# Performance work log

Measured on AMD Instinct MI355X. Metric: run time of the kernel, lower is better.

## Reference

```python
import jax, jax.numpy as jnp
import numpy as np
import math

B, L, H, N, OUT, NPRED, NCTRL = 16, 4096, 512, 64, 256, 128, 64


def setup_inputs() -> dict:
    key = jax.random.key(0)
    ks = jax.random.split(key, 12)
    Nh = N // 2
    inp = jax.random.normal(ks[0], (B, L, H), dtype=jnp.float32)
    spec = jax.random.normal(ks[1], (B, L, NCTRL), dtype=jnp.float32)
    # S4DKernel params
    C = jax.random.normal(ks[2], (H, Nh, 2), dtype=jnp.float32)  # view_as_real of cfloat C
    log_dt = (jax.random.uniform(ks[3], (H,), dtype=jnp.float32)
              * (math.log(0.1) - math.log(0.001)) + math.log(0.001))
    log_A_real = jnp.log(0.5 * jnp.ones((H, Nh), dtype=jnp.float32))
    A_imag = math.pi * jnp.broadcast_to(jnp.arange(Nh, dtype=jnp.float32), (H, Nh))
    D = jax.random.normal(ks[4], (H,), dtype=jnp.float32)
    # output_linear: Conv1d(H, 2H, 1) then GLU(dim=-2)
    conv_w = jax.random.normal(ks[5], (2 * H, H), dtype=jnp.float32) / np.sqrt(H)
    conv_b = jax.random.normal(ks[6], (2 * H,), dtype=jnp.float32) * 0.01
    # output: Linear(in_len, out_len) applied on length axis
    out_w = jax.random.normal(ks[7], (OUT, L), dtype=jnp.float32) / np.sqrt(L)
    out_b = jax.random.normal(ks[8], (OUT,), dtype=jnp.float32) * 0.01
    return {"inp": inp, "spec": spec, "C": C, "log_dt": log_dt,
            "log_A_real": log_A_real, "A_imag": A_imag, "D": D,
            "conv_w": conv_w, "conv_b": conv_b, "out_w": out_w, "out_b": out_b}


def s4d_kernel(C, log_dt, log_A_real, A_imag, L):
    # Materialize SSM convolution kernel K: (H, L)
    dt = jnp.exp(log_dt)                                  # (H,)
    Cc = C[..., 0] + 1j * C[..., 1]                       # (H, N/2) complex
    A = -jnp.exp(log_A_real) + 1j * A_imag                # (H, N/2)
    dtA = A * dt[:, None]                                 # (H, N/2)
    # Vandermonde: exp(dtA * l) for l in [0, L)
    V = jnp.exp(dtA[:, :, None] * jnp.arange(L, dtype=jnp.float32))  # (H, N/2, L)
    Cc = Cc * (jnp.exp(dtA) - 1.0) / A                    # (H, N/2)
    K = 2.0 * jnp.einsum('hn,hnl->hl', Cc, V).real        # (H, L)
    return K


def reference(inp, spec, C, log_dt, log_A_real, A_imag, D, conv_w, conv_b, out_w, out_b):
    x = jnp.swapaxes(inp, -1, -2)                         # (B, H, L)
    Lx = x.shape[-1]
    k = s4d_kernel(C, log_dt, log_A_real, A_imag, Lx)     # (H, L)
    # FFT long convolution (linear conv via zero-padding to 2L)
    k_f = jnp.fft.rfft(k, n=2 * Lx)                       # (H, L+1)
    x_f = jnp.fft.rfft(x, n=2 * Lx)                       # (B, H, L+1)
    y = jnp.fft.irfft(x_f * k_f, n=2 * Lx)[..., :Lx]      # (B, H, L)
    y = y + x * D[:, None]                                # skip connection
    y = jax.nn.gelu(y, approximate=False)                 # torch nn.GELU default (erf)
    # Conv1d(k=1) + GLU over channel dim
    z = jnp.einsum('oh,bhl->bol', conv_w, y) + conv_b[:, None]  # (B, 2H, L)
    a, b = z[:, :H, :], z[:, H:, :]
    y = a * jax.nn.sigmoid(b)                             # (B, H, L)
    # Linear over length axis: L -> OUT
    y = jnp.einsum('bhl,ol->bho', y, out_w) + out_b       # (B, H, OUT)
    y = jnp.swapaxes(y, -1, -2)                           # (B, OUT, H)
    return y[:, :OUT, -NPRED:]
```

## Files before the change

kernel.cpp:

```cpp
#include <hip/hip_runtime.h>
#include <hip/hip_bf16.h>
#include <math.h>

#define B_     16
#define L_     4096
#define H_     512
#define NH     32
#define OUT_   256
#define NPRED_ 128
#define CCH    8
#define LCH    512

typedef __attribute__((ext_vector_type(8))) short bf16x8;
typedef __attribute__((ext_vector_type(4))) float f32x4;
typedef __attribute__((ext_vector_type(2))) float f32x2;

__global__ void prep_kernel(const float* __restrict__ conv_w, const float* __restrict__ conv_b,
                            const float* __restrict__ out_w,
                            __hip_bfloat16* __restrict__ Wsel, float* __restrict__ bselp,
                            __hip_bfloat16* __restrict__ outw)
{
    int idx = blockIdx.x * blockDim.x + threadIdx.x;
    if (idx < 256 * 512) {
        int r = idx >> 9, hcol = idx & 511;
        int src = (r < 128) ? (384 + r) : (768 + r);
        Wsel[idx] = __float2bfloat16(conv_w[src * H_ + hcol]);
    } else if (idx < 256 * 512 + 256 * 4096) {
        int i2 = idx - 256 * 512;
        outw[i2] = __float2bfloat16(out_w[i2]);
    } else if (idx < 256 * 512 + 256 * 4096 + 256) {
        int r = idx - 256 * 512 - 256 * 4096;
        int src = (r < 128) ? (384 + r) : (768 + r);
        bselp[r] = conv_b[src];
    }
}

__global__ __launch_bounds__(256)
void scan_pass1(const float* __restrict__ inp, const float* __restrict__ log_dt,
                const float* __restrict__ log_A_real, const float* __restrict__ A_imag,
                float2* __restrict__ M)
{
    const int b = blockIdx.x, hg = blockIdx.y, cq = blockIdx.z;
    const int tid = threadIdx.x;
    const int wv = tid >> 6, lane = tid & 63;
    const int c = cq * 4 + wv;
    const int hl = lane & 15, nb = (lane >> 4) * 8;
    const int h = hg * 16 + hl;

    f32x2 WR[4], WI[4], WIN[4], SR[4], SI[4];
    const float dt = expf(log_dt[h]);
#pragma unroll
    for (int g = 0; g < 4; ++g) {
#pragma unroll
        for (int e = 0; e < 2; ++e) {
            const int n = nb + g * 2 + e;
            const float Ar = -expf(log_A_real[h * NH + n]);
            const float Ai = A_imag[h * NH + n];
            const float er = expf(Ar * dt);
            WR[g][e] = er * cosf(Ai * dt);
            WI[g][e] = er * sinf(Ai * dt);
            WIN[g][e] = -WI[g][e];
        }
        SR[g] = (f32x2){0.f, 0.f};
        SI[g] = (f32x2){0.f, 0.f};
    }

    const float* xp = inp + ((size_t)b * L_ + (size_t)c * LCH) * H_ + h;
    float xq0 = xp[0 * (size_t)H_];
    float xq1 = xp[1 * (size_t)H_];
    float xq2 = xp[2 * (size_t)H_];
    float xq3 = xp[3 * (size_t)H_];

#define P1_STEP(XV)                                                            \
    {                                                                          \
        const f32x2 X = (f32x2){(XV), (XV)};                                   \
        _Pragma("unroll")                                                      \
        for (int g = 0; g < 4; ++g) {                                          \
            f32x2 t   = __builtin_elementwise_fma(WIN[g], SI[g], X);           \
            f32x2 nSR = __builtin_elementwise_fma(WR[g], SR[g], t);            \
            f32x2 u   = WI[g] * SR[g];                                         \
            f32x2 nSI = __builtin_elementwise_fma(WR[g], SI[g], u);            \
            SR[g] = nSR; SI[g] = nSI;                                          \
        }                                                                      \
    }

#pragma unroll 4
    for (int l = 0; l < LCH - 4; ++l) {
        const float xf = xp[(size_t)(l + 4) * H_];
        P1_STEP(xq0);
        xq0 = xq1; xq1 = xq2; xq2 = xq3; xq3 = xf;
    }
#pragma unroll
    for (int l = LCH - 4; l < LCH; ++l) {
        P1_STEP(xq0);
        xq0 = xq1; xq1 = xq2; xq2 = xq3;
    }
#undef P1_STEP

    float2* Mp = M + (((size_t)b * CCH + c) * H_ + h) * NH + nb;
#pragma unroll
    for (int g = 0; g < 4; ++g) {
        float4 v; v.x = SR[g][0]; v.y = SI[g][0]; v.z = SR[g][1]; v.w = SI[g][1];
        *(float4*)&Mp[g * 2] = v;
    }
}

__global__ __launch_bounds__(256)
void scan_pass2(const float* __restrict__ log_dt, const float* __restrict__ log_A_real,
                const float* __restrict__ A_imag, float2* __restrict__ M)
{
    const int idx = blockIdx.x * 256 + threadIdx.x;
    const int n = idx & 31, h = (idx >> 5) & 511, b = idx >> 14;
    const float dt = expf(log_dt[h]);
    const float Ar = -expf(log_A_real[h * NH + n]);
    const float Ai = A_imag[h * NH + n];
    const float er = expf(Ar * dt);
    float wr = er * cosf(Ai * dt), wi = er * sinf(Ai * dt);
#pragma unroll
    for (int s = 0; s < 9; ++s) {
        float nr = wr * wr - wi * wi;
        float ni = 2.0f * wr * wi;
        wr = nr; wi = ni;
    }
    float sre = 0.f, sim = 0.f;
#pragma unroll
    for (int c = 0; c < CCH; ++c) {
        const size_t mi_ = (((size_t)b * CCH + c) * H_ + h) * NH + n;
        float2 m = M[mi_];
        M[mi_] = make_float2(sre, sim);
        float nr = fmaf(wr, sre, fmaf(-wi, sim, m.x));
        float ni = fmaf(wr, sim, fmaf(wi, sre, m.y));
        sre = nr; sim = ni;
    }
}

__global__ __launch_bounds__(256)
void scan_pass3(const float* __restrict__ inp, const float* __restrict__ C,
                const float* __restrict__ log_dt, const float* __restrict__ log_A_real,
                const float* __restrict__ A_imag, const float* __restrict__ Dv,
                const float2* __restrict__ Sin, __hip_bfloat16* __restrict__ gT)
{
    const int b = blockIdx.x, hg = blockIdx.y, cq = blockIdx.z;
    const int tid = threadIdx.x;
    const int wv = tid >> 6, lane = tid & 63;
    const int c = cq * 4 + wv;
    const int hl = lane & 15, nb = (lane >> 4) * 8;
    const int h = hg * 16 + hl;

    f32x2 WR[4], WI[4], WIN[4], CR[4], CNI[4], SR[4], SI[4];
    const float dt = expf(log_dt[h]);
    const float2* Sp = Sin + (((size_t)b * CCH + c) * H_ + h) * NH + nb;
#pragma unroll
    for (int g = 0; g < 4; ++g) {
#pragma unroll
        for (int e = 0; e < 2; ++e) {
            const int n = nb + g * 2 + e;
            const float Ar = -expf(log_A_real[h * NH + n]);
            const float Ai = A_imag[h * NH + n];
            const float er = expf(Ar * dt);
            const float wrr = er * cosf(Ai * dt);
            const float wii = er * sinf(Ai * dt);
            const float m2 = Ar * Ar + Ai * Ai;
            const float nr = wrr - 1.0f, nim = wii;
            const float qr = (nr * Ar + nim * Ai) / m2;
            const float qi = (nim * Ar - nr * Ai) / m2;
            const float Crv = C[(h * NH + n) * 2 + 0];
            const float Civ = C[(h * NH + n) * 2 + 1];
            WR[g][e] = wrr;  WI[g][e] = wii;  WIN[g][e] = -wii;
            CR[g][e]  =  2.0f * (Crv * qr - Civ * qi);
            CNI[g][e] = -2.0f * (Crv * qi + Civ * qr);
            float2 sv = Sp[g * 2 + e];
            SR[g][e] = sv.x; SI[g][e] = sv.y;
        }
    }
    const float Dh = Dv[h];

    const float* xp = inp + ((size_t)b * L_ + (size_t)c * LCH) * H_ + h;
    __hip_bfloat16* gp = gT + ((size_t)b * L_ + (size_t)c * LCH) * H_ + h;

    float xq0 = xp[0 * (size_t)H_];
    float xq1 = xp[1 * (size_t)H_];
    float xq2 = xp[2 * (size_t)H_];
    float xq3 = xp[3 * (size_t)H_];

#define P3_STEP(LV, XV)                                                        \
    {                                                                          \
        const f32x2 X = (f32x2){(XV), (XV)};                                   \
        f32x2 yp = (f32x2){0.f, 0.f};                                          \
        _Pragma("unroll")                                                      \
        for (int g = 0; g < 4; ++g) {                                          \
            f32x2 t   = __builtin_elementwise_fma(WIN[g], SI[g], X);           \
            f32x2 nSR = __builtin_elementwise_fma(WR[g], SR[g], t);            \
            f32x2 u   = WI[g] * SR[g];                                         \
            f32x2 nSI = __builtin_elementwise_fma(WR[g], SI[g], u);            \
            SR[g] = nSR; SI[g] = nSI;                                          \
            yp = __builtin_elementwise_fma(CR[g], nSR, yp);                    \
            yp = __builtin_elementwise_fma(CNI[g], nSI, yp);                   \
        }                                                                      \
        float y = yp[0] + yp[1];                                               \
        y += __shfl_xor(y, 16);                                                \
        y += __shfl_xor(y, 32);                                                \
        const float v = fmaf(Dh, (XV), y);                                     \
        float u2 = v * fmaf(0.0356774081f, v * v, 0.797884561f);               \
        u2 = fmaxf(u2, -15.0f);                                                \
        const float e2 = __expf(-2.0f * u2);                                   \
        const float th = 1.0f - 2.0f * e2 * __builtin_amdgcn_rcpf(1.0f + e2);  \
        const float ge = 0.5f * v * (1.0f + th);                               \
        if (lane < 16) gp[(size_t)(LV) * H_] = __float2bfloat16(ge);           \
    }

#pragma unroll 2
    for (int l = 0; l < LCH - 4; ++l) {
        const float xf = xp[(size_t)(l + 4) * H_];
        P3_STEP(l, xq0);
        xq0 = xq1; xq1 = xq2; xq2 = xq3; xq3 = xf;
    }
#pragma unroll
    for (int l = LCH - 4; l < LCH; ++l) {
        P3_STEP(l, xq0);
        xq0 = xq1; xq1 = xq2; xq2 = xq3;
    }
#undef P3_STEP
}

__device__ __forceinline__ unsigned short bf16bits(float f) {
    __hip_bfloat16 hv = __float2bfloat16(f);
    return *reinterpret_cast<unsigned short*>(&hv);
}

__global__ __launch_bounds__(512)
void gemm1_kernel(const __hip_bfloat16* __restrict__ gT, const __hip_bfloat16* __restrict__ Wsel,
                  const float* __restrict__ bsel, __hip_bfloat16* __restrict__ gated)
{
    const int b  = blockIdx.y;
    const int l0 = blockIdx.x * 128;
    const int tid = threadIdx.x;
    const int wid = tid >> 6, lane = tid & 63;
    const int wrr = wid >> 2;
    const int wcc = wid & 3;
    const int lr  = lane & 15;
    const int lk8 = (lane >> 4) * 8;

    __shared__ short As[128][40];
    __shared__ short Bs[256][40];

    f32x4 acc[4][4];
#pragma unroll
    for (int i = 0; i < 4; ++i)
#pragma unroll
        for (int j = 0; j < 4; ++j) acc[i][j] = (f32x4){0.f, 0.f, 0.f, 0.f};

    const short* gsrc = (const short*)gT + ((size_t)b * L_ + l0) * H_;
    const short* wsrc = (const short*)Wsel;
    const int arow = tid >> 2, aseg = tid & 3;

    for (int ks = 0; ks < 16; ++ks) {
        const int k0 = ks * 32;
        uint4 av  = *(const uint4*)(gsrc + (size_t)arow * H_ + k0 + aseg * 8);
        uint4 bv0 = *(const uint4*)(wsrc + (size_t)arow * 512 + k0 + aseg * 8);
        uint4 bv1 = *(const uint4*)(wsrc + (size_t)(arow + 128) * 512 + k0 + aseg * 8);
        *(uint4*)&As[arow][aseg * 8]       = av;
        *(uint4*)&Bs[arow][aseg * 8]       = bv0;
        *(uint4*)&Bs[arow + 128][aseg * 8] = bv1;
        __syncthreads();

        bf16x8 af[4], bfr[4];
#pragma unroll
        for (int mi = 0; mi < 4; ++mi)
            af[mi] = *(const bf16x8*)&As[wrr * 64 + mi * 16 + lr][lk8];
#pragma unroll
        for (int ni = 0; ni < 4; ++ni) {
            int col = (ni < 2) ? (wcc * 32 + ni * 16) : (128 + wcc * 32 + (ni - 2) * 16);
            bfr[ni] = *(const bf16x8*)&Bs[col + lr][lk8];
        }
#pragma unroll
        for (int mi = 0; mi < 4; ++mi)
#pragma unroll
            for (int ni = 0; ni < 4; ++ni)
                acc[mi][ni] = __builtin_amdgcn_mfma_f32_16x16x32_bf16(af[mi], bfr[ni], acc[mi][ni], 0, 0, 0);
        __syncthreads();
    }

    const int lj4 = (lane >> 4) * 4;
#pragma unroll
    for (int mi = 0; mi < 4; ++mi) {
#pragma unroll
        for (int ni = 0; ni < 2; ++ni) {
            const int oa = wcc * 32 + ni * 16 + lr;
            const float ba  = bsel[oa];
            const float bbv = bsel[oa + 128];
            ushort4 pack;
            unsigned short* pu = (unsigned short*)&pack;
#pragma unroll
            for (int j = 0; j < 4; ++j) {
                float za = acc[mi][ni][j] + ba;
                float zb = acc[mi][ni + 2][j] + bbv;
                float gv = za * (1.0f / (1.0f + expf(-zb)));
                pu[j] = bf16bits(gv);
            }
            const int lrow = l0 + wrr * 64 + mi * 16 + lj4;
            *(ushort4*)((unsigned short*)gated + ((size_t)b * NPRED_ + oa) * L_ + lrow) = pack;
        }
    }
}

__global__ __launch_bounds__(256)
void gemm2_kernel(const __hip_bfloat16* __restrict__ gated, const __hip_bfloat16* __restrict__ outw,
                  const float* __restrict__ outb, float* __restrict__ outp)
{
    const int b  = blockIdx.y;
    const int ot = blockIdx.x & 3, ht = blockIdx.x >> 2;
    const int o0 = ot * 64, hh0 = ht * 64;
    const int tid = threadIdx.x;
    const int wid = tid >> 6, lane = tid & 63;
    const int wrr = wid >> 1;
    const int wcc = wid & 1;
    const int lr  = lane & 15;
    const int lk8 = (lane >> 4) * 8;

    __shared__ short As[64][72];
    __shared__ short Bs[64][72];

    f32x4 acc[2][2];
#pragma unroll
    for (int i = 0; i < 2; ++i)
#pragma unroll
        for (int j = 0; j < 2; ++j) acc[i][j] = (f32x4){0.f, 0.f, 0.f, 0.f};

    const short* asrc = (const short*)gated + ((size_t)b * NPRED_ + hh0) * L_;
    const short* bsrc = (const short*)outw + (size_t)o0 * L_;
    const int row = tid >> 2, seg = tid & 3;

    for (int ks = 0; ks < 64; ++ks) {
        const int k0 = ks * 64;
        uint4 a0 = *(const uint4*)(asrc + (size_t)row * L_ + k0 + seg * 8);
        uint4 a1 = *(const uint4*)(asrc + (size_t)row * L_ + k0 + 32 + seg * 8);
        uint4 b0 = *(const uint4*)(bsrc + (size_t)row * L_ + k0 + seg * 8);
        uint4 b1 = *(const uint4*)(bsrc + (size_t)row * L_ + k0 + 32 + seg * 8);
        __syncthreads();
        *(uint4*)&As[row][seg * 8]      = a0;
        *(uint4*)&As[row][32 + seg * 8] = a1;
        *(uint4*)&Bs[row][seg * 8]      = b0;
        *(uint4*)&Bs[row][32 + seg * 8] = b1;
        __syncthreads();

#pragma unroll
        for (int kk = 0; kk < 2; ++kk) {
            bf16x8 af[2], bfv[2];
#pragma unroll
            for (int mi = 0; mi < 2; ++mi)
                af[mi] = *(const bf16x8*)&As[wrr * 32 + mi * 16 + lr][kk * 32 + lk8];
#pragma unroll
            for (int ni = 0; ni < 2; ++ni)
                bfv[ni] = *(const bf16x8*)&Bs[wcc * 32 + ni * 16 + lr][kk * 32 + lk8];
#pragma unroll
            for (int mi = 0; mi < 2; ++mi)
#pragma unroll
                for (int ni = 0; ni < 2; ++ni)
                    acc[mi][ni] = __builtin_amdgcn_mfma_f32_16x16x32_bf16(af[mi], bfv[ni], acc[mi][ni], 0, 0, 0);
        }
    }

    const int lj4 = (lane >> 4) * 4;
#pragma unroll
    for (int mi = 0; mi < 2; ++mi) {
#pragma unroll
        for (int ni = 0; ni < 2; ++ni) {
            const int og = o0 + wcc * 32 + ni * 16 + lr;
            const float bo = outb[og];
            float4 v;
            v.x = acc[mi][ni][0] + bo;
            v.y = acc[mi][ni][1] + bo;
            v.z = acc[mi][ni][2] + bo;
            v.w = acc[mi][ni][3] + bo;
            const int hh = hh0 + wrr * 32 + mi * 16 + lj4;
            *(float4*)(outp + ((size_t)b * OUT_ + og) * NPRED_ + hh) = v;
        }
    }
}

extern "C" void kernel_launch(void* const* d_in, const int* in_sizes, int n_in,
                              void* d_out, int out_size, void* d_ws, size_t ws_size,
                              hipStream_t stream)
{
    const float* inp        = (const float*)d_in[0];
    const float* C          = (const float*)d_in[2];
    const float* log_dt     = (const float*)d_in[3];
    const float* log_A_real = (const float*)d_in[4];
    const float* A_imag     = (const float*)d_in[5];
    const float* Dv         = (const float*)d_in[6];
    const float* conv_w     = (const float*)d_in[7];
    const float* conv_b     = (const float*)d_in[8];
    const float* out_w      = (const float*)d_in[9];
    const float* out_b      = (const float*)d_in[10];
    float* outp = (float*)d_out;

    const size_t off_Wsel  = 0;
    const size_t off_outw  = 262144;
    const size_t off_bsel  = 2359296;
    const size_t off_gT    = 2360320;
    const size_t off_gated = 69469184;
    const size_t off_M     = off_gated;
    const size_t need      = 86246400;
    if (ws_size < need) return;

    char* ws = (char*)d_ws;
    __hip_bfloat16* Wsel  = (__hip_bfloat16*)(ws + off_Wsel);
    __hip_bfloat16* outw  = (__hip_bfloat16*)(ws + off_outw);
    float*          bselp = (float*)(ws + off_bsel);
    __hip_bfloat16* gT    = (__hip_bfloat16*)(ws + off_gT);
    __hip_bfloat16* gated = (__hip_bfloat16*)(ws + off_gated);
    float2*         M     = (float2*)(ws + off_M);

    const int prep_total = 256 * 512 + 256 * 4096 + 256;
    prep_kernel<<<(prep_total + 255) / 256, 256, 0, stream>>>(conv_w, conv_b, out_w, Wsel, bselp, outw);
    scan_pass1<<<dim3(16, 32, 2), 256, 0, stream>>>(inp, log_dt, log_A_real, A_imag, M);
    scan_pass2<<<1024, 256, 0, stream>>>(log_dt, log_A_real, A_imag, M);
    scan_pass3<<<dim3(16, 32, 2), 256, 0, stream>>>(inp, C, log_dt, log_A_real, A_imag, Dv, M, gT);
    gemm1_kernel<<<dim3(32, 16), 512, 0, stream>>>(gT, Wsel, bselp, gated);
    gemm2_kernel<<<dim3(8, 16), 256, 0, stream>>>(gated, outw, out_b, outp);
}
```

Baseline: 580.3 us.

## Force packed FMA via inline asm and block scan steps with distributed GELU epilogue

Rewrites the inner recurrence of scan passes 1 and 3 to use inline-asm v_pk_fma_f32/v_pk_mul_f32 so the compiler cannot scalarize the packed complex updates. The input stream is now prefetched in blocks of 8 timesteps into registers instead of a 4-deep rolling queue. In pass 3, the cross-lane shuffle reductions are batched over 8 steps, and the GELU epilogue and stores are spread across all four 16-lane groups (each handling two timesteps) rather than only lane<16 doing the work. The cost is higher register pressure from the 16 buffered inputs and 8 partial sums, plus inline asm that hides instructions from the compiler's scheduler.

```diff
diff --git a/kernel.cpp b/kernel.cpp
--- a/kernel.cpp
+++ b/kernel.cpp
@@ -14,6 +14,10 @@
 typedef __attribute__((ext_vector_type(8))) short bf16x8;
 typedef __attribute__((ext_vector_type(4))) float f32x4;
 typedef __attribute__((ext_vector_type(2))) float f32x2;
+
+#define PKFMA(D, A, Bv, Cv) asm("v_pk_fma_f32 %0, %1, %2, %3" : "=v"(D) : "v"(A), "v"(Bv), "v"(Cv))
+#define PKFMA_ACC(D, A, Bv) asm("v_pk_fma_f32 %0, %1, %2, %0" : "+v"(D) : "v"(A), "v"(Bv))
+#define PKMUL(D, A, Bv)     asm("v_pk_mul_f32 %0, %1, %2" : "=v"(D) : "v"(A), "v"(Bv))
 
 __global__ void prep_kernel(const float* __restrict__ conv_w, const float* __restrict__ conv_b,
                             const float* __restrict__ out_w,
@@ -66,34 +70,34 @@
     }
 
     const float* xp = inp + ((size_t)b * L_ + (size_t)c * LCH) * H_ + h;
-    float xq0 = xp[0 * (size_t)H_];
-    float xq1 = xp[1 * (size_t)H_];
-    float xq2 = xp[2 * (size_t)H_];
-    float xq3 = xp[3 * (size_t)H_];
+
+    float xc[8], xn[8];
+#pragma unroll
+    for (int i = 0; i < 8; ++i) xc[i] = xp[(size_t)i * H_];
 
 #define P1_STEP(XV)                                                            \
     {                                                                          \
-        const f32x2 X = (f32x2){(XV), (XV)};                                   \
+        f32x2 X; X[0] = (XV); X[1] = (XV);                                     \
         _Pragma("unroll")                                                      \
         for (int g = 0; g < 4; ++g) {                                          \
-            f32x2 t   = __builtin_elementwise_fma(WIN[g], SI[g], X);           \
-            f32x2 nSR = __builtin_elementwise_fma(WR[g], SR[g], t);            \
-            f32x2 u   = WI[g] * SR[g];                                         \
-            f32x2 nSI = __builtin_elementwise_fma(WR[g], SI[g], u);            \
+            f32x2 t1, t2, nSR, nSI;                                            \
+            PKFMA(t1, WIN[g], SI[g], X);                                       \
+            PKFMA(nSR, WR[g], SR[g], t1);                                      \
+            PKMUL(t2, WI[g], SR[g]);                                           \
+            PKFMA(nSI, WR[g], SI[g], t2);                                      \
             SR[g] = nSR; SI[g] = nSI;                                          \
         }                                                                      \
     }
 
-#pragma unroll 4
-    for (int l = 0; l < LCH - 4; ++l) {
-        const float xf = xp[(size_t)(l + 4) * H_];
-        P1_STEP(xq0);
-        xq0 = xq1; xq1 = xq2; xq2 = xq3; xq3 = xf;
-    }
-#pragma unroll
-    for (int l = LCH - 4; l < LCH; ++l) {
-        P1_STEP(xq0);
-        xq0 = xq1; xq1 = xq2; xq2 = xq3;
+    for (int blk = 0; blk < 64; ++blk) {
+        if (blk < 63) {
+#pragma unroll
+            for (int i = 0; i < 8; ++i) xn[i] = xp[(size_t)(blk * 8 + 8 + i) * H_];
+        }
+#pragma unroll
+        for (int s = 0; s < 8; ++s) P1_STEP(xc[s]);
+#pragma unroll
+        for (int i = 0; i < 8; ++i) xc[i] = xn[i];
     }
 #undef P1_STEP
 
@@ -146,6 +150,9 @@
     const int c = cq * 4 + wv;
     const int hl = lane & 15, nb = (lane >> 4) * 8;
     const int h = hg * 16 + hl;
+    const bool pb0 = ((lane >> 4) & 1) != 0;
+    const bool pb1 = ((lane >> 4) & 2) != 0;
+    const int p = lane >> 4;
 
     f32x2 WR[4], WI[4], WIN[4], CR[4], CNI[4], SR[4], SI[4];
     const float dt = expf(log_dt[h]);
@@ -178,49 +185,60 @@
     const float* xp = inp + ((size_t)b * L_ + (size_t)c * LCH) * H_ + h;
     __hip_bfloat16* gp = gT + ((size_t)b * L_ + (size_t)c * LCH) * H_ + h;
 
-    float xq0 = xp[0 * (size_t)H_];
-    float xq1 = xp[1 * (size_t)H_];
-    float xq2 = xp[2 * (size_t)H_];
-    float xq3 = xp[3 * (size_t)H_];
-
-#define P3_STEP(LV, XV)                                                        \
-    {                                                                          \
-        const f32x2 X = (f32x2){(XV), (XV)};                                   \
-        f32x2 yp = (f32x2){0.f, 0.f};                                          \
-        _Pragma("unroll")                                                      \
-        for (int g = 0; g < 4; ++g) {                                          \
-            f32x2 t   = __builtin_elementwise_fma(WIN[g], SI[g], X);           \
-            f32x2 nSR = __builtin_elementwise_fma(WR[g], SR[g], t);            \
-            f32x2 u   = WI[g] * SR[g];                                         \
-            f32x2 nSI = __builtin_elementwise_fma(WR[g], SI[g], u);            \
-            SR[g] = nSR; SI[g] = nSI;                                          \
-            yp = __builtin_elementwise_fma(CR[g], nSR, yp);                    \
-            yp = __builtin_elementwise_fma(CNI[g], nSI, yp);                   \
-        }                                                                      \
-        float y = yp[0] + yp[1];                                               \
-        y += __shfl_xor(y, 16);                                                \
-        y += __shfl_xor(y, 32);                                                \
-        const float v = fmaf(Dh, (XV), y);                                     \
-        float u2 = v * fmaf(0.0356774081f, v * v, 0.797884561f);               \
-        u2 = fmaxf(u2, -15.0f);                                                \
-        const float e2 = __expf(-2.0f * u2);                                   \
-        const float th = 1.0f - 2.0f * e2 * __builtin_amdgcn_rcpf(1.0f + e2);  \
-        const float ge = 0.5f * v * (1.0f + th);                               \
-        if (lane < 16) gp[(size_t)(LV) * H_] = __float2bfloat16(ge);           \
-    }
-
-#pragma unroll 2
-    for (int l = 0; l < LCH - 4; ++l) {
-        const float xf = xp[(size_t)(l + 4) * H_];
-        P3_STEP(l, xq0);
-        xq0 = xq1; xq1 = xq2; xq2 = xq3; xq3 = xf;
-    }
-#pragma unroll
-    for (int l = LCH - 4; l < LCH; ++l) {
-        P3_STEP(l, xq0);
-        xq0 = xq1; xq1 = xq2; xq2 = xq3;
-    }
-#undef P3_STEP
+    float xc[8], xn[8];
+#pragma unroll
+    for (int i = 0; i < 8; ++i) xc[i] = xp[(size_t)i * H_];
+
+    for (int blk = 0; blk < 64; ++blk) {
+        if (blk < 63) {
+#pragma unroll
+            for (int i = 0; i < 8; ++i) xn[i] = xp[(size_t)(blk * 8 + 8 + i) * H_];
+        }
+        float y8[8];
+#pragma unroll
+        for (int s = 0; s < 8; ++s) {
+            f32x2 X; X[0] = xc[s]; X[1] = xc[s];
+            f32x2 yp;
+#pragma unroll
+            for (int g = 0; g < 4; ++g) {
+                f32x2 t1, t2, nSR, nSI;
+                PKFMA(t1, WIN[g], SI[g], X);
+                PKFMA(nSR, WR[g], SR[g], t1);
+                PKMUL(t2, WI[g], SR[g]);
+                PKFMA(nSI, WR[g], SI[g], t2);
+                SR[g] = nSR; SI[g] = nSI;
+                if (g == 0) {
+                    PKMUL(yp, CR[0], nSR);
+                } else {
+                    PKFMA_ACC(yp, CR[g], nSR);
+                }
+                PKFMA_ACC(yp, CNI[g], nSI);
+            }
+            y8[s] = yp[0] + yp[1];
+        }
+#pragma unroll
+        for (int s = 0; s < 8; ++s) y8[s] += __shfl_xor(y8[s], 16);
+#pragma unroll
+        for (int s = 0; s < 8; ++s) y8[s] += __shfl_xor(y8[s], 32);
+#pragma unroll
+        for (int e = 0; e < 2; ++e) {
+            const float ys = e == 0
+                ? (pb1 ? (pb0 ? y8[6] : y8[4]) : (pb0 ? y8[2] : y8[0]))
+                : (pb1 ? (pb0 ? y8[7] : y8[5]) : (pb0 ? y8[3] : y8[1]));
+            const float xs = e == 0
+                ? (pb1 ? (pb0 ? xc[6] : xc[4]) : (pb0 ? xc[2] : xc[0]))
+                : (pb1 ? (pb0 ? xc[7] : xc[5]) : (pb0 ? xc[3] : xc[1]));
+            const float v = fmaf(Dh, xs, ys);
+            float u2 = v * fmaf(0.0356774081f, v * v, 0.797884561f);
+            u2 = fmaxf(u2, -15.0f);
+            const float e2 = __expf(-2.0f * u2);
+            const float th = 1.0f - 2.0f * e2 * __builtin_amdgcn_rcpf(1.0f + e2);
+            const float ge = 0.5f * v * (1.0f + th);
+            gp[(size_t)(blk * 8 + p * 2 + e) * H_] = __float2bfloat16(ge);
+        }
+#pragma unroll
+        for (int i = 0; i < 8; ++i) xc[i] = xn[i];
+    }
 }
 
 __device__ __forceinline__ unsigned short bf16bits(float f) {
```

After: 545.6 us. 6.0% less time.
